# Kernel optimization log

Hardware: AMD Instinct MI355X
Metric: run time of the kernel (lower is better)

## Reference

```python
import jax, jax.numpy as jnp
import numpy as np

# STN forward: grid = reference_ijk_grid + ddf (voxel units); the module then
# normalizes each axis to [-1,1] with align_corners=True and reverses axis order
# for F.grid_sample. Under align_corners=True the normalize->denormalize round
# trip is the identity, so the sample locations are exactly ref+ddf in voxel
# coordinates per (d,h,w) axis. padding_mode='border' => clamp coords to the
# valid range before trilinear interpolation.

def _grid_sample_3d_border(image, ddf):
    # image: [B,C,D,H,W], ddf: [B,3,D,H,W] (voxel-space displacements in d,h,w order)
    B, C, D, H, W = image.shape
    dt = image.dtype
    ref = jnp.stack(
        jnp.meshgrid(jnp.arange(D, dtype=dt), jnp.arange(H, dtype=dt),
                     jnp.arange(W, dtype=dt), indexing='ij'), axis=0)  # [3,D,H,W]
    coords = ref[None] + ddf  # [B,3,D,H,W] absolute voxel coords

    def sample_one(img, c):  # img [C,D,H,W], c [3,D,H,W]
        cd = jnp.clip(c[0], 0.0, D - 1.0)  # border padding: clamp coord
        ch = jnp.clip(c[1], 0.0, H - 1.0)
        cw = jnp.clip(c[2], 0.0, W - 1.0)
        d0 = jnp.floor(cd); h0 = jnp.floor(ch); w0 = jnp.floor(cw)
        fd = cd - d0; fh = ch - h0; fw = cw - w0  # [D,H,W] fractional weights
        d0i = d0.astype(jnp.int32); h0i = h0.astype(jnp.int32); w0i = w0.astype(jnp.int32)
        d1i = jnp.minimum(d0i + 1, D - 1)
        h1i = jnp.minimum(h0i + 1, H - 1)
        w1i = jnp.minimum(w0i + 1, W - 1)

        def g(di, hi, wi):  # gather 1 corner for all channels -> [C,D,H,W]
            return img[:, di, hi, wi]

        out = (g(d0i, h0i, w0i) * ((1 - fd) * (1 - fh) * (1 - fw))
             + g(d0i, h0i, w1i) * ((1 - fd) * (1 - fh) * fw)
             + g(d0i, h1i, w0i) * ((1 - fd) * fh * (1 - fw))
             + g(d0i, h1i, w1i) * ((1 - fd) * fh * fw)
             + g(d1i, h0i, w0i) * (fd * (1 - fh) * (1 - fw))
             + g(d1i, h0i, w1i) * (fd * (1 - fh) * fw)
             + g(d1i, h1i, w0i) * (fd * fh * (1 - fw))
             + g(d1i, h1i, w1i) * (fd * fh * fw))
        return out

    return jax.vmap(sample_one)(image, coords)  # [B,C,D,H,W]


def setup_inputs() -> dict:
    key = jax.random.key(0)
    k1, k2 = jax.random.split(key)
    image = jax.random.normal(k1, (2, 2, 128, 128, 128), dtype=jnp.float32)
    ddf = jax.random.normal(k2, (2, 3, 128, 128, 128), dtype=jnp.float32)
    return {"image": image, "ddf": ddf}


def reference(image, ddf):
    return _grid_sample_3d_border(image, ddf)
```

## Files before the change

kernel.cpp:

```cpp
#include <hip/hip_runtime.h>


constexpr int B = 2, C = 2, D = 128, H = 128, W = 128;
constexpr int HW  = H * W;
constexpr int DHW = D * HW;
constexpr int RDH = 11;
constexpr int RWD = 40;
constexpr int NROW = RDH * RDH;
constexpr int NROW_P = 128;
constexpr int LDSF = NROW_P * RWD;
constexpr int NG = LDSF / 4;
constexpr int NT = 256;
constexpr int ROW_B = RWD * 4;
constexpr int PLANE_B = RDH * ROW_B;

typedef float v2f __attribute__((ext_vector_type(2)));

__device__ __forceinline__ void gload_lds16(const float* g, float* l) {
    __builtin_amdgcn_global_load_lds(
        (const __attribute__((address_space(1))) void*)g,
        (__attribute__((address_space(3))) void*)l, 16, 0, 0);
}

__global__ __launch_bounds__(NT) void stn_kernel(
    const float* __restrict__ image,
    const float* __restrict__ ddf,
    float* __restrict__ out)
{
    __shared__ float smem[LDSF];

    const int bid = blockIdx.x;
    const int cpx = gridDim.x >> 3;
    const int blk = (bid & 7) * cpx + (bid >> 3);

    const int b   = blk >> 12;
    const int tb  = blk & 4095;
    const int t0d = (tb >> 7) * 4;
    const int t0h = ((tb >> 2) & 31) * 4;
    const int t0w = (tb & 3) * 32;
    const int lo_d = max(t0d - 3, 0), lo_h = max(t0h - 3, 0);
    const int lo_w = max(t0w - 4, 0);
    const int hi_d = min(lo_d + RDH - 1, D - 1);
    const int hi_h = min(lo_h + RDH - 1, H - 1);
    const int hi_w = min(lo_w + RWD - 1, W - 1);
    const float* imgb = image + (size_t)b * C * DHW;
    const int tid = threadIdx.x;
    const unsigned lds0 =
        (unsigned)(uintptr_t)(__attribute__((address_space(3))) void*)&smem[0];

    const int dd = tid >> 6, hh = (tid >> 4) & 3, wi = tid & 15;
    const int d_ = t0d + dd, h_ = t0h + hh;
    const int w2 = t0w + wi * 2;
    const int sidx = d_ * HW + h_ * W + w2;

    const float* dp = ddf + (size_t)b * 3 * DHW;
    float2 vd = *reinterpret_cast<const float2*>(dp + sidx);
    float2 vh = *reinterpret_cast<const float2*>(dp + DHW + sidx);
    float2 vw = *reinterpret_cast<const float2*>(dp + 2 * DHW + sidx);
    asm volatile("" ::: "memory");

    auto gsrc_off = [&](int g) {
        int row = g / 10;
        int rw  = (g - row * 10) * 4;
        int rc  = min(row, NROW - 1);
        int rd  = rc / RDH;
        int rh  = rc - rd * RDH;
        return min(lo_d + rd, D - 1) * HW + min(lo_h + rh, H - 1) * W
             + min(lo_w + rw, W - 4);
    };

    auto issue_stage = [&](const float* src) {
#pragma unroll
        for (int i = 0; i < 5; ++i) {
            int g = tid + i * NT;
            gload_lds16(src + gsrc_off(g), &smem[g * 4]);
        }
    };

    issue_stage(imgb);
    asm volatile("" ::: "memory");

    float cds[2], chs[2], cws[2];
    cds[0] = fminf(fmaxf((float)d_ + vd.x, 0.0f), (float)(D - 1));
    cds[1] = fminf(fmaxf((float)d_ + vd.y, 0.0f), (float)(D - 1));
    chs[0] = fminf(fmaxf((float)h_ + vh.x, 0.0f), (float)(H - 1));
    chs[1] = fminf(fmaxf((float)h_ + vh.y, 0.0f), (float)(H - 1));
    cws[0] = fminf(fmaxf((float)w2 + vw.x, 0.0f), (float)(W - 1));
    cws[1] = fminf(fmaxf((float)(w2 + 1) + vw.y, 0.0f), (float)(W - 1));

    auto do_pass = [&](const float* gimg, float* optr) {
        unsigned a0[2];
        float W00[2], W01[2], W10[2], W11[2], GD[2], FD[2];
        int fb = 0;
#pragma unroll
        for (int k = 0; k < 2; ++k) {
            float cd = cds[k], ch = chs[k], cw = cws[k];
            float d0f = floorf(cd), h0f = floorf(ch), w0f = floorf(cw);
            float fd = cd - d0f, fh = ch - h0f, fw = cw - w0f;
            int d0 = (int)d0f, h0 = (int)h0f, w0 = (int)w0f;
            bool bad = (d0 < lo_d) | (d0 + 1 > hi_d)
                     | (h0 < lo_h) | (h0 + 1 > hi_h)
                     | (w0 < lo_w) | (w0 + 1 > hi_w);
            fb |= (int)bad << k;
            float gh = 1.0f - fh, gw = 1.0f - fw;
            W00[k] = gh * gw; W01[k] = gh * fw;
            W10[k] = fh * gw; W11[k] = fh * fw;
            GD[k] = 1.0f - fd; FD[k] = fd;
            int row = (d0 - lo_d) * RDH + (h0 - lo_h);
            a0[k] = lds0 + (unsigned)(row * ROW_B + (w0 - lo_w) * 4);
        }
        v2f r00[2], r01[2], r10[2], r11[2];
#pragma unroll
        for (int k = 0; k < 2; ++k) {
            unsigned a1 = a0[k] + PLANE_B;
            asm volatile("ds_read2_b32 %0, %1 offset0:0 offset1:1"
                         : "=v"(r00[k]) : "v"(a0[k]));
            asm volatile("ds_read2_b32 %0, %1 offset0:40 offset1:41"
                         : "=v"(r01[k]) : "v"(a0[k]));
            asm volatile("ds_read2_b32 %0, %1 offset0:0 offset1:1"
                         : "=v"(r10[k]) : "v"(a1));
            asm volatile("ds_read2_b32 %0, %1 offset0:40 offset1:41"
                         : "=v"(r11[k]) : "v"(a1));
        }
        asm volatile("s_waitcnt lgkmcnt(0)" ::: "memory");
        __builtin_amdgcn_sched_barrier(0);

        float acc[2];
#pragma unroll
        for (int k = 0; k < 2; ++k) {
            float p0 = r00[k].x * W00[k] + r00[k].y * W01[k]
                     + r01[k].x * W10[k] + r01[k].y * W11[k];
            float p1 = r10[k].x * W00[k] + r10[k].y * W01[k]
                     + r11[k].x * W10[k] + r11[k].y * W11[k];
            acc[k] = GD[k] * p0 + FD[k] * p1;
        }
        if (fb) {
#pragma unroll
            for (int k = 0; k < 2; ++k) {
                if (fb & (1 << k)) {
                    float cd = cds[k], ch = chs[k], cw = cws[k];
                    float d0f = floorf(cd), h0f = floorf(ch), w0f = floorf(cw);
                    float fd = cd - d0f, fh = ch - h0f, fw = cw - w0f;
                    int d0 = (int)d0f, h0 = (int)h0f, w0 = (int)w0f;
                    int d1 = min(d0 + 1, D - 1);
                    int h1 = min(h0 + 1, H - 1);
                    int w1 = min(w0 + 1, W - 1);
                    float gd = 1.0f - fd, gh = 1.0f - fh, gw = 1.0f - fw;
                    float w00 = gh * gw, w01 = gh * fw, w10 = fh * gw, w11 = fh * fw;
                    int o00 = d0 * HW + h0 * W, o01 = d0 * HW + h1 * W;
                    int o10 = d1 * HW + h0 * W, o11 = d1 * HW + h1 * W;
                    float q0 = gimg[o00 + w0] * w00 + gimg[o00 + w1] * w01
                             + gimg[o01 + w0] * w10 + gimg[o01 + w1] * w11;
                    float q1 = gimg[o10 + w0] * w00 + gimg[o10 + w1] * w01
                             + gimg[o11 + w0] * w10 + gimg[o11 + w1] * w11;
                    acc[k] = gd * q0 + fd * q1;
                }
            }
        }
        *reinterpret_cast<float2*>(optr) = make_float2(acc[0], acc[1]);
    };

    float* outb = out + (size_t)b * C * DHW;

    asm volatile("s_waitcnt vmcnt(0)" ::: "memory");
    __builtin_amdgcn_s_barrier();
    do_pass(imgb, outb + sidx);

    __builtin_amdgcn_s_barrier();
    asm volatile("" ::: "memory");

    issue_stage(imgb + DHW);
    asm volatile("s_waitcnt vmcnt(0)" ::: "memory");
    __builtin_amdgcn_s_barrier();
    do_pass(imgb + DHW, outb + DHW + sidx);
}

extern "C" void kernel_launch(void* const* d_in, const int* in_sizes, int n_in,
                              void* d_out, int out_size, void* d_ws, size_t ws_size,
                              hipStream_t stream) {
    const float* image = (const float*)d_in[0];
    const float* ddf   = (const float*)d_in[1];
    float* out = (float*)d_out;

    int grid = B * 4096;
    stn_kernel<<<grid, NT, 0, stream>>>(image, ddf, out);
}
```

Before: 37.64 us.

## Shrink output tile to 4x4x16 with one voxel per thread and smaller halo

Each block now covers a 4x4x16 output tile with one voxel per thread instead of a 4x4x32 tile with two voxels per thread. The LDS halo window shrinks to 11x11x28 floats per channel, filled with four 16-byte direct-to-LDS loads per thread instead of five, and the grid doubles. The aim is less LDS use and more resident blocks per CU to hide latency. The cost is a higher halo-to-output ratio, which means more total image traffic, plus narrower ddf and output accesses.

```diff
diff --git a/kernel.cpp b/kernel.cpp
--- a/kernel.cpp
+++ b/kernel.cpp
@@ -5,13 +5,12 @@
 constexpr int HW  = H * W;
 constexpr int DHW = D * HW;
 constexpr int RDH = 11;
-constexpr int RWD = 40;
-constexpr int NROW = RDH * RDH;
-constexpr int NROW_P = 128;
-constexpr int LDSF = NROW_P * RWD;
-constexpr int NG = LDSF / 4;
+constexpr int ROWD = 28;
+constexpr int NROWR = 121;
+constexpr int GPR = 7;
+constexpr int NG = 1024;
 constexpr int NT = 256;
-constexpr int ROW_B = RWD * 4;
+constexpr int ROW_B = ROWD * 4;
 constexpr int PLANE_B = RDH * ROW_B;
 
 typedef float v2f __attribute__((ext_vector_type(2)));
@@ -27,42 +26,41 @@
     const float* __restrict__ ddf,
     float* __restrict__ out)
 {
-    __shared__ float smem[LDSF];
+    __shared__ float smem[NG * 4];
 
     const int bid = blockIdx.x;
     const int cpx = gridDim.x >> 3;
     const int blk = (bid & 7) * cpx + (bid >> 3);
 
-    const int b   = blk >> 12;
-    const int tb  = blk & 4095;
-    const int t0d = (tb >> 7) * 4;
-    const int t0h = ((tb >> 2) & 31) * 4;
-    const int t0w = (tb & 3) * 32;
+    const int b  = blk >> 13;
+    const int tb = blk & 8191;
+    const int t0d = (tb >> 8) * 4;
+    const int t0h = ((tb >> 3) & 31) * 4;
+    const int t0w = (tb & 7) * 16;
     const int lo_d = max(t0d - 3, 0), lo_h = max(t0h - 3, 0);
     const int lo_w = max(t0w - 4, 0);
     const int hi_d = min(lo_d + RDH - 1, D - 1);
     const int hi_h = min(lo_h + RDH - 1, H - 1);
-    const int hi_w = min(lo_w + RWD - 1, W - 1);
+    const int hi_w = min(lo_w + 23, W - 1);
     const float* imgb = image + (size_t)b * C * DHW;
     const int tid = threadIdx.x;
     const unsigned lds0 =
         (unsigned)(uintptr_t)(__attribute__((address_space(3))) void*)&smem[0];
 
-    const int dd = tid >> 6, hh = (tid >> 4) & 3, wi = tid & 15;
-    const int d_ = t0d + dd, h_ = t0h + hh;
-    const int w2 = t0w + wi * 2;
-    const int sidx = d_ * HW + h_ * W + w2;
+    const int dd = tid >> 6, hh = (tid >> 4) & 3, wl = tid & 15;
+    const int d_ = t0d + dd, h_ = t0h + hh, w_ = t0w + wl;
+    const int sidx = d_ * HW + h_ * W + w_;
 
     const float* dp = ddf + (size_t)b * 3 * DHW;
-    float2 vd = *reinterpret_cast<const float2*>(dp + sidx);
-    float2 vh = *reinterpret_cast<const float2*>(dp + DHW + sidx);
-    float2 vw = *reinterpret_cast<const float2*>(dp + 2 * DHW + sidx);
+    float vdd = dp[sidx];
+    float vhh = dp[DHW + sidx];
+    float vww = dp[2 * DHW + sidx];
     asm volatile("" ::: "memory");
 
     auto gsrc_off = [&](int g) {
-        int row = g / 10;
-        int rw  = (g - row * 10) * 4;
-        int rc  = min(row, NROW - 1);
+        int row = g / GPR;
+        int rw  = (g - row * GPR) * 4;
+        int rc  = min(row, NROWR - 1);
         int rd  = rc / RDH;
         int rh  = rc - rd * RDH;
         return min(lo_d + rd, D - 1) * HW + min(lo_h + rh, H - 1) * W
@@ -71,7 +69,7 @@
 
     auto issue_stage = [&](const float* src) {
 #pragma unroll
-        for (int i = 0; i < 5; ++i) {
+        for (int i = 0; i < 4; ++i) {
             int g = tid + i * NT;
             gload_lds16(src + gsrc_off(g), &smem[g * 4]);
         }
@@ -80,84 +78,51 @@
     issue_stage(imgb);
     asm volatile("" ::: "memory");
 
-    float cds[2], chs[2], cws[2];
-    cds[0] = fminf(fmaxf((float)d_ + vd.x, 0.0f), (float)(D - 1));
-    cds[1] = fminf(fmaxf((float)d_ + vd.y, 0.0f), (float)(D - 1));
-    chs[0] = fminf(fmaxf((float)h_ + vh.x, 0.0f), (float)(H - 1));
-    chs[1] = fminf(fmaxf((float)h_ + vh.y, 0.0f), (float)(H - 1));
-    cws[0] = fminf(fmaxf((float)w2 + vw.x, 0.0f), (float)(W - 1));
-    cws[1] = fminf(fmaxf((float)(w2 + 1) + vw.y, 0.0f), (float)(W - 1));
+    float cd = fminf(fmaxf((float)d_ + vdd, 0.0f), (float)(D - 1));
+    float ch = fminf(fmaxf((float)h_ + vhh, 0.0f), (float)(H - 1));
+    float cw = fminf(fmaxf((float)w_ + vww, 0.0f), (float)(W - 1));
+    float d0f = floorf(cd), h0f = floorf(ch), w0f = floorf(cw);
+    float FD = cd - d0f, FH = ch - h0f, FW = cw - w0f;
+    float GD = 1.0f - FD, GHt = 1.0f - FH, GWt = 1.0f - FW;
+    int d0 = (int)d0f, h0 = (int)h0f, w0 = (int)w0f;
+    const bool bad = (d0 < lo_d) | (d0 + 1 > hi_d)
+                   | (h0 < lo_h) | (h0 + 1 > hi_h)
+                   | (w0 < lo_w) | (w0 + 1 > hi_w);
+    float W00 = GHt * GWt, W01 = GHt * FW, W10 = FH * GWt, W11 = FH * FW;
+    const unsigned a0 = lds0 +
+        (unsigned)(((d0 - lo_d) * RDH + (h0 - lo_h)) * ROW_B + (w0 - lo_w) * 4);
+    const unsigned a1 = a0 + PLANE_B;
 
     auto do_pass = [&](const float* gimg, float* optr) {
-        unsigned a0[2];
-        float W00[2], W01[2], W10[2], W11[2], GD[2], FD[2];
-        int fb = 0;
-#pragma unroll
-        for (int k = 0; k < 2; ++k) {
-            float cd = cds[k], ch = chs[k], cw = cws[k];
-            float d0f = floorf(cd), h0f = floorf(ch), w0f = floorf(cw);
-            float fd = cd - d0f, fh = ch - h0f, fw = cw - w0f;
-            int d0 = (int)d0f, h0 = (int)h0f, w0 = (int)w0f;
-            bool bad = (d0 < lo_d) | (d0 + 1 > hi_d)
-                     | (h0 < lo_h) | (h0 + 1 > hi_h)
-                     | (w0 < lo_w) | (w0 + 1 > hi_w);
-            fb |= (int)bad << k;
-            float gh = 1.0f - fh, gw = 1.0f - fw;
-            W00[k] = gh * gw; W01[k] = gh * fw;
-            W10[k] = fh * gw; W11[k] = fh * fw;
-            GD[k] = 1.0f - fd; FD[k] = fd;
-            int row = (d0 - lo_d) * RDH + (h0 - lo_h);
-            a0[k] = lds0 + (unsigned)(row * ROW_B + (w0 - lo_w) * 4);
-        }
-        v2f r00[2], r01[2], r10[2], r11[2];
-#pragma unroll
-        for (int k = 0; k < 2; ++k) {
-            unsigned a1 = a0[k] + PLANE_B;
-            asm volatile("ds_read2_b32 %0, %1 offset0:0 offset1:1"
-                         : "=v"(r00[k]) : "v"(a0[k]));
-            asm volatile("ds_read2_b32 %0, %1 offset0:40 offset1:41"
-                         : "=v"(r01[k]) : "v"(a0[k]));
-            asm volatile("ds_read2_b32 %0, %1 offset0:0 offset1:1"
-                         : "=v"(r10[k]) : "v"(a1));
-            asm volatile("ds_read2_b32 %0, %1 offset0:40 offset1:41"
-                         : "=v"(r11[k]) : "v"(a1));
-        }
+        v2f r00, r01, r10, r11;
+        asm volatile("ds_read2_b32 %0, %1 offset0:0 offset1:1"
+                     : "=v"(r00) : "v"(a0));
+        asm volatile("ds_read2_b32 %0, %1 offset0:28 offset1:29"
+                     : "=v"(r01) : "v"(a0));
+        asm volatile("ds_read2_b32 %0, %1 offset0:0 offset1:1"
+                     : "=v"(r10) : "v"(a1));
+        asm volatile("ds_read2_b32 %0, %1 offset0:28 offset1:29"
+                     : "=v"(r11) : "v"(a1));
         asm volatile("s_waitcnt lgkmcnt(0)" ::: "memory");
         __builtin_amdgcn_sched_barrier(0);
 
-        float acc[2];
-#pragma unroll
-        for (int k = 0; k < 2; ++k) {
-            float p0 = r00[k].x * W00[k] + r00[k].y * W01[k]
-                     + r01[k].x * W10[k] + r01[k].y * W11[k];
-            float p1 = r10[k].x * W00[k] + r10[k].y * W01[k]
-                     + r11[k].x * W10[k] + r11[k].y * W11[k];
-            acc[k] = GD[k] * p0 + FD[k] * p1;
+        float p0 = r00.x * W00 + r00.y * W01 + r01.x * W10 + r01.y * W11;
+        float p1 = r10.x * W00 + r10.y * W01 + r11.x * W10 + r11.y * W11;
+        float acc = GD * p0 + FD * p1;
+
+        if (bad) {
+            int d1i = min(d0 + 1, D - 1);
+            int h1i = min(h0 + 1, H - 1);
+            int w1i = min(w0 + 1, W - 1);
+            int o00 = d0 * HW + h0 * W, o01 = d0 * HW + h1i * W;
+            int o10 = d1i * HW + h0 * W, o11 = d1i * HW + h1i * W;
+            float q0 = gimg[o00 + w0] * W00 + gimg[o00 + w1i] * W01
+                     + gimg[o01 + w0] * W10 + gimg[o01 + w1i] * W11;
+            float q1 = gimg[o10 + w0] * W00 + gimg[o10 + w1i] * W01
+                     + gimg[o11 + w0] * W10 + gimg[o11 + w1i] * W11;
+            acc = GD * q0 + FD * q1;
         }
-        if (fb) {
-#pragma unroll
-            for (int k = 0; k < 2; ++k) {
-                if (fb & (1 << k)) {
-                    float cd = cds[k], ch = chs[k], cw = cws[k];
-                    float d0f = floorf(cd), h0f = floorf(ch), w0f = floorf(cw);
-                    float fd = cd - d0f, fh = ch - h0f, fw = cw - w0f;
-                    int d0 = (int)d0f, h0 = (int)h0f, w0 = (int)w0f;
-                    int d1 = min(d0 + 1, D - 1);
-                    int h1 = min(h0 + 1, H - 1);
-                    int w1 = min(w0 + 1, W - 1);
-                    float gd = 1.0f - fd, gh = 1.0f - fh, gw = 1.0f - fw;
-                    float w00 = gh * gw, w01 = gh * fw, w10 = fh * gw, w11 = fh * fw;
-                    int o00 = d0 * HW + h0 * W, o01 = d0 * HW + h1 * W;
-                    int o10 = d1 * HW + h0 * W, o11 = d1 * HW + h1 * W;
-                    float q0 = gimg[o00 + w0] * w00 + gimg[o00 + w1] * w01
-                             + gimg[o01 + w0] * w10 + gimg[o01 + w1] * w11;
-                    float q1 = gimg[o10 + w0] * w00 + gimg[o10 + w1] * w01
-                             + gimg[o11 + w0] * w10 + gimg[o11 + w1] * w11;
-                    acc[k] = gd * q0 + fd * q1;
-                }
-            }
-        }
-        *reinterpret_cast<float2*>(optr) = make_float2(acc[0], acc[1]);
+        *optr = acc;
     };
 
     float* outb = out + (size_t)b * C * DHW;
@@ -182,6 +147,6 @@
     const float* ddf   = (const float*)d_in[1];
     float* out = (float*)d_out;
 
-    int grid = B * 4096;
+    int grid = B * 8192;
     stn_kernel<<<grid, NT, 0, stream>>>(image, ddf, out);
 }
```

New measurement: 42.54 us. 1.13x slower.

## Double output tile height and pad LDS rows to 44 floats

Applied to the files above, without the earlier changes.

Each block now covers a 4x8x32 output tile with 512 threads instead of 4x4x32 with 256, and stages an 11x15x44 halo region in LDS (rows padded from 40 to 44 floats). The larger tile lowers the halo-to-interior ratio, so fewer redundant global loads go into LDS per output. The coordinate, weight and address setup is hoisted out of the per-channel pass so it is computed once. In exchange the block and LDS footprint grow, which may reduce occupancy, and the row padding changes the LDS bank mapping.

```diff
diff --git a/kernel.cpp b/kernel.cpp
--- a/kernel.cpp
+++ b/kernel.cpp
@@ -4,15 +4,14 @@
 constexpr int B = 2, C = 2, D = 128, H = 128, W = 128;
 constexpr int HW  = H * W;
 constexpr int DHW = D * HW;
-constexpr int RDH = 11;
-constexpr int RWD = 40;
-constexpr int NROW = RDH * RDH;
-constexpr int NROW_P = 128;
-constexpr int LDSF = NROW_P * RWD;
-constexpr int NG = LDSF / 4;
-constexpr int NT = 256;
-constexpr int ROW_B = RWD * 4;
-constexpr int PLANE_B = RDH * ROW_B;
+constexpr int RD = 11, RH = 15;
+constexpr int ROWD = 44;
+constexpr int GPR = 11;
+constexpr int NROWR = RD * RH;
+constexpr int NG = 2048;
+constexpr int NT = 512;
+constexpr int ROW_B = ROWD * 4;
+constexpr int PLANE_B = RH * ROW_B;
 
 typedef float v2f __attribute__((ext_vector_type(2)));
 
@@ -27,28 +26,28 @@
     const float* __restrict__ ddf,
     float* __restrict__ out)
 {
-    __shared__ float smem[LDSF];
+    __shared__ float smem[NG * 4];
 
     const int bid = blockIdx.x;
     const int cpx = gridDim.x >> 3;
     const int blk = (bid & 7) * cpx + (bid >> 3);
 
-    const int b   = blk >> 12;
-    const int tb  = blk & 4095;
-    const int t0d = (tb >> 7) * 4;
-    const int t0h = ((tb >> 2) & 31) * 4;
+    const int b  = blk >> 11;
+    const int tb = blk & 2047;
+    const int t0d = (tb >> 6) * 4;
+    const int t0h = ((tb >> 2) & 15) * 8;
     const int t0w = (tb & 3) * 32;
     const int lo_d = max(t0d - 3, 0), lo_h = max(t0h - 3, 0);
     const int lo_w = max(t0w - 4, 0);
-    const int hi_d = min(lo_d + RDH - 1, D - 1);
-    const int hi_h = min(lo_h + RDH - 1, H - 1);
-    const int hi_w = min(lo_w + RWD - 1, W - 1);
+    const int hi_d = min(lo_d + RD - 1, D - 1);
+    const int hi_h = min(lo_h + RH - 1, H - 1);
+    const int hi_w = min(lo_w + 39, W - 1);
     const float* imgb = image + (size_t)b * C * DHW;
     const int tid = threadIdx.x;
     const unsigned lds0 =
         (unsigned)(uintptr_t)(__attribute__((address_space(3))) void*)&smem[0];
 
-    const int dd = tid >> 6, hh = (tid >> 4) & 3, wi = tid & 15;
+    const int dd = tid >> 7, hh = (tid >> 4) & 7, wi = tid & 15;
     const int d_ = t0d + dd, h_ = t0h + hh;
     const int w2 = t0w + wi * 2;
     const int sidx = d_ * HW + h_ * W + w2;
@@ -60,18 +59,18 @@
     asm volatile("" ::: "memory");
 
     auto gsrc_off = [&](int g) {
-        int row = g / 10;
-        int rw  = (g - row * 10) * 4;
-        int rc  = min(row, NROW - 1);
-        int rd  = rc / RDH;
-        int rh  = rc - rd * RDH;
+        int row = g / GPR;
+        int rw  = (g - row * GPR) * 4;
+        int rc  = min(row, NROWR - 1);
+        int rd  = rc / RH;
+        int rh  = rc - rd * RH;
         return min(lo_d + rd, D - 1) * HW + min(lo_h + rh, H - 1) * W
              + min(lo_w + rw, W - 4);
     };
 
     auto issue_stage = [&](const float* src) {
 #pragma unroll
-        for (int i = 0; i < 5; ++i) {
+        for (int i = 0; i < 4; ++i) {
             int g = tid + i * NT;
             gload_lds16(src + gsrc_off(g), &smem[g * 4]);
         }
@@ -88,38 +87,39 @@
     cws[0] = fminf(fmaxf((float)w2 + vw.x, 0.0f), (float)(W - 1));
     cws[1] = fminf(fmaxf((float)(w2 + 1) + vw.y, 0.0f), (float)(W - 1));
 
+    unsigned a0[2];
+    float W00[2], W01[2], W10[2], W11[2], GD[2], FD[2];
+    int fb = 0;
+#pragma unroll
+    for (int k = 0; k < 2; ++k) {
+        float cd = cds[k], ch = chs[k], cw = cws[k];
+        float d0f = floorf(cd), h0f = floorf(ch), w0f = floorf(cw);
+        float fd = cd - d0f, fh = ch - h0f, fw = cw - w0f;
+        int d0 = (int)d0f, h0 = (int)h0f, w0 = (int)w0f;
+        bool bad = (d0 < lo_d) | (d0 + 1 > hi_d)
+                 | (h0 < lo_h) | (h0 + 1 > hi_h)
+                 | (w0 < lo_w) | (w0 + 1 > hi_w);
+        fb |= (int)bad << k;
+        float gh = 1.0f - fh, gw = 1.0f - fw;
+        W00[k] = gh * gw; W01[k] = gh * fw;
+        W10[k] = fh * gw; W11[k] = fh * fw;
+        GD[k] = 1.0f - fd; FD[k] = fd;
+        int row = (d0 - lo_d) * RH + (h0 - lo_h);
+        a0[k] = lds0 + (unsigned)(row * ROW_B + (w0 - lo_w) * 4);
+    }
+
     auto do_pass = [&](const float* gimg, float* optr) {
-        unsigned a0[2];
-        float W00[2], W01[2], W10[2], W11[2], GD[2], FD[2];
-        int fb = 0;
-#pragma unroll
-        for (int k = 0; k < 2; ++k) {
-            float cd = cds[k], ch = chs[k], cw = cws[k];
-            float d0f = floorf(cd), h0f = floorf(ch), w0f = floorf(cw);
-            float fd = cd - d0f, fh = ch - h0f, fw = cw - w0f;
-            int d0 = (int)d0f, h0 = (int)h0f, w0 = (int)w0f;
-            bool bad = (d0 < lo_d) | (d0 + 1 > hi_d)
-                     | (h0 < lo_h) | (h0 + 1 > hi_h)
-                     | (w0 < lo_w) | (w0 + 1 > hi_w);
-            fb |= (int)bad << k;
-            float gh = 1.0f - fh, gw = 1.0f - fw;
-            W00[k] = gh * gw; W01[k] = gh * fw;
-            W10[k] = fh * gw; W11[k] = fh * fw;
-            GD[k] = 1.0f - fd; FD[k] = fd;
-            int row = (d0 - lo_d) * RDH + (h0 - lo_h);
-            a0[k] = lds0 + (unsigned)(row * ROW_B + (w0 - lo_w) * 4);
-        }
         v2f r00[2], r01[2], r10[2], r11[2];
 #pragma unroll
         for (int k = 0; k < 2; ++k) {
             unsigned a1 = a0[k] + PLANE_B;
             asm volatile("ds_read2_b32 %0, %1 offset0:0 offset1:1"
                          : "=v"(r00[k]) : "v"(a0[k]));
-            asm volatile("ds_read2_b32 %0, %1 offset0:40 offset1:41"
+            asm volatile("ds_read2_b32 %0, %1 offset0:44 offset1:45"
                          : "=v"(r01[k]) : "v"(a0[k]));
             asm volatile("ds_read2_b32 %0, %1 offset0:0 offset1:1"
                          : "=v"(r10[k]) : "v"(a1));
-            asm volatile("ds_read2_b32 %0, %1 offset0:40 offset1:41"
+            asm volatile("ds_read2_b32 %0, %1 offset0:44 offset1:45"
                          : "=v"(r11[k]) : "v"(a1));
         }
         asm volatile("s_waitcnt lgkmcnt(0)" ::: "memory");
@@ -182,6 +182,6 @@
     const float* ddf   = (const float*)d_in[1];
     float* out = (float*)d_out;
 
-    int grid = B * 4096;
+    int grid = B * 2048;
     stn_kernel<<<grid, NT, 0, stream>>>(image, ddf, out);
 }
```

New measurement: 35.30 us. -6.2%, faster.
